# Kernel optimization log

Hardware: AMD Instinct MI355X
Metric: run time of the kernel (lower is better)

Reference implementation:

```python
import jax, jax.numpy as jnp
import numpy as np

TAU = 0.5
EPS = 1e-8


def setup_inputs() -> dict:
    key = jax.random.key(0)
    k1, k2 = jax.random.split(key)
    N, D = 200000, 512
    z_pos = jax.random.normal(k1, (N, D), dtype=jnp.float32)
    W = jax.random.normal(k2, (D, D), dtype=jnp.float32) * (1.0 / np.sqrt(D))
    b = jnp.zeros((D,), dtype=jnp.float32)
    return {"z_pos": z_pos, "W": W, "b": b}


def reference(z_pos, W, b):
    # sample_centroid: softmax-weighted centroid (computed on detached embeddings)
    h = jax.lax.stop_gradient(z_pos)
    init_c = h.mean(axis=0)                              # [D]
    d2 = jnp.sum((h - init_c[None, :]) ** 2, axis=1)     # [N]
    w = jax.nn.softmax(-d2 / TAU)                        # [N]
    c = jnp.sum(h * w[:, None], axis=0)                  # [D]

    # SimNet: dist = 1 - cosine_similarity(proj(x), c)
    x_proj = z_pos @ W.T + b                             # [N, D]
    x_norm = jnp.maximum(jnp.linalg.norm(x_proj, axis=-1), EPS)  # [N]
    c_norm = jnp.maximum(jnp.linalg.norm(c), EPS)
    cos = (x_proj @ c) / (x_norm * c_norm)               # [N]
    dist = 1.0 - cos
    return dist
```

## Files before the change

### kernel.cpp

```cpp
#include <hip/hip_runtime.h>
#include <hip/hip_bf16.h>
#include <math.h>

#define DD 512
#define EPSF 1e-8f
#define BM 128
#define BK 32
#define FBIG 3.402823466e+38f

typedef __bf16 bf16_t;
typedef __bf16 bf16x4 __attribute__((ext_vector_type(4)));
typedef __bf16 bf16x8 __attribute__((ext_vector_type(8)));
typedef float f32x4 __attribute__((ext_vector_type(4)));

__global__ void k_convW(const float* __restrict__ W, bf16_t* __restrict__ Wb) {
    int i = blockIdx.x * blockDim.x + threadIdx.x;
    float4 v = ((const float4*)W)[i];
    bf16x4 o;
    o[0] = (bf16_t)v.x; o[1] = (bf16_t)v.y; o[2] = (bf16_t)v.z; o[3] = (bf16_t)v.w;
    ((bf16x4*)Wb)[i] = o;
}

__global__ void k_colsum(const float* __restrict__ z, float* __restrict__ part, int N) {
    int t = threadIdx.x;
    int b = blockIdx.x;
    int col4 = t & 127, sub = t >> 7;
    const float4* z4 = (const float4*)z;
    float4 acc = make_float4(0.f, 0.f, 0.f, 0.f);
    int npair = (N + 1) >> 1;
    #pragma unroll 2
    for (int p = b; p < npair; p += gridDim.x) {
        int r = p * 2 + sub;
        if (r < N) {
            float4 v = z4[(size_t)r * 128 + col4];
            acc.x += v.x; acc.y += v.y; acc.z += v.z; acc.w += v.w;
        }
    }
    __shared__ float4 sm[128];
    if (sub == 1) sm[col4] = acc;
    __syncthreads();
    if (sub == 0) {
        float4 o = sm[col4];
        acc.x += o.x; acc.y += o.y; acc.z += o.z; acc.w += o.w;
        ((float4*)(part + (size_t)b * DD))[col4] = acc;
    }
}

__global__ void k_wcolsum(const float* __restrict__ z, const float* __restrict__ d2,
                          const float* __restrict__ d2min, const float* __restrict__ sinvp,
                          float* __restrict__ part, int N) {
    int t = threadIdx.x;
    int b = blockIdx.x;
    int col4 = t & 127, sub = t >> 7;
    float m  = d2min[0];
    float is = sinvp[0];
    const float4* z4 = (const float4*)z;
    float4 acc = make_float4(0.f, 0.f, 0.f, 0.f);
    int npair = (N + 1) >> 1;
    #pragma unroll 2
    for (int p = b; p < npair; p += gridDim.x) {
        int r = p * 2 + sub;
        if (r < N) {
            float w = __expf(-2.0f * (d2[r] - m)) * is;
            float4 v = z4[(size_t)r * 128 + col4];
            acc.x += w * v.x; acc.y += w * v.y; acc.z += w * v.z; acc.w += w * v.w;
        }
    }
    __shared__ float4 sm[128];
    if (sub == 1) sm[col4] = acc;
    __syncthreads();
    if (sub == 0) {
        float4 o = sm[col4];
        acc.x += o.x; acc.y += o.y; acc.z += o.z; acc.w += o.w;
        ((float4*)(part + (size_t)b * DD))[col4] = acc;
    }
}

__global__ void k_reduce1024(const float* __restrict__ part, float* __restrict__ outv, float scale) {
    __shared__ float sm[256];
    int j = blockIdx.x;
    int t = threadIdx.x;
    float s = part[(size_t)t * DD + j] + part[(size_t)(t + 256) * DD + j]
            + part[(size_t)(t + 512) * DD + j] + part[(size_t)(t + 768) * DD + j];
    sm[t] = s;
    __syncthreads();
    for (int st = 128; st > 0; st >>= 1) {
        if (t < st) sm[t] += sm[t + st];
        __syncthreads();
    }
    if (t == 0) outv[j] = sm[0] * scale;
}

__global__ void k_d2s(const float* __restrict__ z, const float* __restrict__ cbar,
                      float* __restrict__ d2, float* __restrict__ mpart,
                      float* __restrict__ spart, int N) {
    int lane = threadIdx.x & 63;
    int wvid = threadIdx.x >> 6;
    int gw = (blockIdx.x * blockDim.x + threadIdx.x) >> 6;
    int nw = (gridDim.x * blockDim.x) >> 6;
    const float4* c4 = (const float4*)cbar;
    float4 ca = c4[lane];
    float4 cb = c4[lane + 64];
    float m = FBIG, s = 0.f;
    for (int r = gw; r < N; r += nw) {
        const float4* zr = (const float4*)(z + (size_t)r * DD);
        float4 a  = zr[lane];
        float4 bb = zr[lane + 64];
        float d, sum = 0.f;
        d = a.x  - ca.x; sum += d * d;
        d = a.y  - ca.y; sum += d * d;
        d = a.z  - ca.z; sum += d * d;
        d = a.w  - ca.w; sum += d * d;
        d = bb.x - cb.x; sum += d * d;
        d = bb.y - cb.y; sum += d * d;
        d = bb.z - cb.z; sum += d * d;
        d = bb.w - cb.w; sum += d * d;
        #pragma unroll
        for (int off = 1; off < 64; off <<= 1) sum += __shfl_xor(sum, off, 64);
        if (lane == 0) d2[r] = sum;
        float nm = fminf(m, sum);
        s = s * __expf(-2.0f * (m - nm)) + __expf(-2.0f * (sum - nm));
        m = nm;
    }
    __shared__ float smm[4], sms[4];
    if (lane == 0) { smm[wvid] = m; sms[wvid] = s; }
    __syncthreads();
    if (threadIdx.x == 0) {
        float M = smm[0];
        M = fminf(M, smm[1]); M = fminf(M, smm[2]); M = fminf(M, smm[3]);
        float S = 0.f;
        #pragma unroll
        for (int i = 0; i < 4; ++i) S += sms[i] * __expf(-2.0f * (smm[i] - M));
        mpart[blockIdx.x] = M;
        spart[blockIdx.x] = S;
    }
}

__global__ void k_combine(const float* __restrict__ mpart, const float* __restrict__ spart,
                          float* __restrict__ d2min, float* __restrict__ sinvp) {
    __shared__ float smm[256], sms[256];
    int t = threadIdx.x;
    float M = FBIG, S = 0.f;
    for (int i = t; i < 1024; i += 256) {
        float m2 = mpart[i], s2 = spart[i];
        float nm = fminf(M, m2);
        S = S * __expf(-2.0f * (M - nm)) + s2 * __expf(-2.0f * (m2 - nm));
        M = nm;
    }
    smm[t] = M; sms[t] = S;
    __syncthreads();
    for (int st = 128; st > 0; st >>= 1) {
        if (t < st) {
            float m2 = smm[t + st], s2 = sms[t + st];
            float nm = fminf(smm[t], m2);
            sms[t] = sms[t] * __expf(-2.0f * (smm[t] - nm)) + s2 * __expf(-2.0f * (m2 - nm));
            smm[t] = nm;
        }
        __syncthreads();
    }
    if (t == 0) { d2min[0] = smm[0]; sinvp[0] = 1.0f / sms[0]; }
}

__global__ void k_cnorm(const float* __restrict__ cvec, float* __restrict__ outp) {
    __shared__ float sm[512];
    float v = cvec[threadIdx.x];
    sm[threadIdx.x] = v * v;
    __syncthreads();
    for (int st = 256; st > 0; st >>= 1) {
        if (threadIdx.x < st) sm[threadIdx.x] += sm[threadIdx.x + st];
        __syncthreads();
    }
    if (threadIdx.x == 0) outp[0] = 1.0f / fmaxf(sqrtf(sm[0]), EPSF);
}

__global__ __launch_bounds__(512, 2) void k_gemm(
    const float* __restrict__ z, const bf16_t* __restrict__ Wb,
    const float* __restrict__ bvec, const float* __restrict__ cvec,
    const float* __restrict__ cninv, float* __restrict__ out, int N)
{
    __shared__ bf16_t As[2][BM * BK];
    __shared__ bf16_t Bs[2][DD * BK];
    __shared__ float psq[BM][4];
    __shared__ float pdt[BM][4];

    const int t    = threadIdx.x;
    const int lane = t & 63;
    const int wv   = t >> 6;
    const int wr   = wv >> 2;
    const int wc   = wv & 3;
    const int quad = lane >> 4;
    const int l15  = lane & 15;
    const int row0 = blockIdx.x * BM;

    const int ai = t >> 2;
    const int ak = (t & 3) * 8;
    const bool arow_ok = (row0 + ai) < N;
    const float4* zrow = (const float4*)(z + (size_t)(row0 + ai) * DD + ak);

    const bf16_t* bsrc = Wb + (size_t)(t >> 2) * DD + (t & 3) * 8;

    f32x4 acc[4][8];
    #pragma unroll
    for (int a = 0; a < 4; ++a)
        #pragma unroll
        for (int b = 0; b < 8; ++b) acc[a][b] = (f32x4){0.f, 0.f, 0.f, 0.f};

    #pragma unroll
    for (int q = 0; q < 4; ++q) {
        int ldsoff = __builtin_amdgcn_readfirstlane(q * 8192 + wv * 1024);
        __builtin_amdgcn_global_load_lds(
            (const __attribute__((address_space(1))) unsigned int*)(const void*)(bsrc + (size_t)q * 128 * DD),
            (__attribute__((address_space(3))) unsigned int*)(void*)((char*)&Bs[0][0] + ldsoff),
            16, 0, 0);
    }
    {
        float4 v0 = make_float4(0.f,0.f,0.f,0.f), v1 = v0;
        if (arow_ok) { v0 = zrow[0]; v1 = zrow[1]; }
        bf16x8 a8;
        a8[0]=(bf16_t)v0.x; a8[1]=(bf16_t)v0.y; a8[2]=(bf16_t)v0.z; a8[3]=(bf16_t)v0.w;
        a8[4]=(bf16_t)v1.x; a8[5]=(bf16_t)v1.y; a8[6]=(bf16_t)v1.z; a8[7]=(bf16_t)v1.w;
        *(bf16x8*)(&As[0][ai * BK + ak]) = a8;
    }
    asm volatile("s_waitcnt vmcnt(0)" ::: "memory");
    __syncthreads();

    #pragma unroll 1
    for (int kc2 = 0; kc2 < 16; ++kc2) {
        const int cur = kc2 & 1;
        const int nxt = cur ^ 1;
        float4 v0 = make_float4(0.f,0.f,0.f,0.f), v1 = v0;
        if (kc2 < 15) {
            const int kc = (kc2 + 1) * BK;
            #pragma unroll
            for (int q = 0; q < 4; ++q) {
                int ldsoff = __builtin_amdgcn_readfirstlane(q * 8192 + wv * 1024);
                __builtin_amdgcn_global_load_lds(
                    (const __attribute__((address_space(1))) unsigned int*)(const void*)(bsrc + (size_t)q * 128 * DD + kc),
                    (__attribute__((address_space(3))) unsigned int*)(void*)((char*)&Bs[nxt][0] + ldsoff),
                    16, 0, 0);
            }
            if (arow_ok) { v0 = zrow[kc >> 2]; v1 = zrow[(kc >> 2) + 1]; }
        }

        bf16x8 af[4];
        #pragma unroll
        for (int rt = 0; rt < 4; ++rt)
            af[rt] = *(const bf16x8*)(&As[cur][(wr * 64 + rt * 16 + l15) * BK + quad * 8]);
        #pragma unroll
        for (int ct = 0; ct < 8; ++ct) {
            bf16x8 bfv = *(const bf16x8*)(&Bs[cur][(wc * 128 + ct * 16 + l15) * BK + quad * 8]);
            #pragma unroll
            for (int rt = 0; rt < 4; ++rt)
                acc[rt][ct] = __builtin_amdgcn_mfma_f32_16x16x32_bf16(af[rt], bfv, acc[rt][ct], 0, 0, 0);
        }

        if (kc2 < 15) {
            bf16x8 a8;
            a8[0]=(bf16_t)v0.x; a8[1]=(bf16_t)v0.y; a8[2]=(bf16_t)v0.z; a8[3]=(bf16_t)v0.w;
            a8[4]=(bf16_t)v1.x; a8[5]=(bf16_t)v1.y; a8[6]=(bf16_t)v1.z; a8[7]=(bf16_t)v1.w;
            *(bf16x8*)(&As[nxt][ai * BK + ak]) = a8;
        }
        asm volatile("s_waitcnt vmcnt(0)" ::: "memory");
        __syncthreads();
    }

    float bc[8], cc[8];
    #pragma unroll
    for (int ct = 0; ct < 8; ++ct) {
        int col = wc * 128 + ct * 16 + l15;
        bc[ct] = bvec[col];
        cc[ct] = cvec[col];
    }
    #pragma unroll
    for (int rt = 0; rt < 4; ++rt) {
        #pragma unroll
        for (int rg = 0; rg < 4; ++rg) {
            float sq = 0.f, dt = 0.f;
            #pragma unroll
            for (int ct = 0; ct < 8; ++ct) {
                float x = acc[rt][ct][rg] + bc[ct];
                sq += x * x;
                dt += x * cc[ct];
            }
            #pragma unroll
            for (int off = 1; off < 16; off <<= 1) {
                sq += __shfl_xor(sq, off, 64);
                dt += __shfl_xor(dt, off, 64);
            }
            if (l15 == 0) {
                int rl = wr * 64 + rt * 16 + quad * 4 + rg;
                psq[rl][wc] = sq;
                pdt[rl][wc] = dt;
            }
        }
    }
    __syncthreads();
    if (t < BM) {
        int r = row0 + t;
        if (r < N) {
            float sq = psq[t][0] + psq[t][1] + psq[t][2] + psq[t][3];
            float dt = pdt[t][0] + pdt[t][1] + pdt[t][2] + pdt[t][3];
            float xi = 1.0f / fmaxf(sqrtf(sq), EPSF);
            out[r] = 1.0f - dt * xi * cninv[0];
        }
    }
}

extern "C" void kernel_launch(void* const* d_in, const int* in_sizes, int n_in,
                              void* d_out, int out_size, void* d_ws, size_t ws_size,
                              hipStream_t stream)
{
    const float* z = (const float*)d_in[0];
    const float* W = (const float*)d_in[1];
    const float* b = (const float*)d_in[2];
    float* out = (float*)d_out;
    int N = in_sizes[0] / DD;

    float* ws = (float*)d_ws;
    size_t off = 0;
    float* part  = ws + off; off += (size_t)1024 * DD;
    float* cbar  = ws + off; off += DD;
    float* d2    = ws + off; off += (size_t)N;
    float* mpart = ws + off; off += 1024;
    float* spart = ws + off; off += 1024;
    float* d2min = ws + off; off += 1;
    float* sinvp = ws + off; off += 1;
    float* cvec  = ws + off; off += DD;
    float* cninv = ws + off; off += 1;
    off = (off + 3) & ~(size_t)3;
    bf16_t* Wb   = (bf16_t*)(ws + off);

    k_convW<<<256, 256, 0, stream>>>(W, Wb);
    k_colsum<<<1024, 256, 0, stream>>>(z, part, N);
    k_reduce1024<<<DD, 256, 0, stream>>>(part, cbar, 1.0f / (float)N);
    k_d2s<<<1024, 256, 0, stream>>>(z, cbar, d2, mpart, spart, N);
    k_combine<<<1, 256, 0, stream>>>(mpart, spart, d2min, sinvp);
    k_wcolsum<<<1024, 256, 0, stream>>>(z, d2, d2min, sinvp, part, N);
    k_reduce1024<<<DD, 256, 0, stream>>>(part, cvec, 1.0f);
    k_cnorm<<<1, DD, 0, stream>>>(cvec, cninv);
    int nblk = (N + BM - 1) / BM;
    k_gemm<<<nblk, 512, 0, stream>>>(z, Wb, b, cvec, cninv, out, N);
}
```

Baseline: 931.4 us.

## Split GEMM over column tiles, add final reduce, contiguous row ranges for reductions

The GEMM now tiles 128x128 output blocks over a 2D grid (4 column tiles) with 256 threads, single-buffered LDS, and writes per-column-tile partial norms and dots that a new final kernel combines. Column-sum kernels process contiguous row chunks per block instead of striding over the grid. The d2 kernel now gives each 16-lane group its own row. Together these aim at better occupancy and memory locality, but each z row is now read and converted four times by the GEMM, and the double buffering is gone.

```diff
diff --git a/kernel.cpp b/kernel.cpp
--- a/kernel.cpp
+++ b/kernel.cpp
@@ -5,8 +5,10 @@
 #define DD 512
 #define EPSF 1e-8f
 #define BM 128
+#define BN 128
 #define BK 32
 #define FBIG 3.402823466e+38f
+#define NPAD 200064
 
 typedef __bf16 bf16_t;
 typedef __bf16 bf16x4 __attribute__((ext_vector_type(4)));
@@ -21,20 +23,17 @@
     ((bf16x4*)Wb)[i] = o;
 }
 
-__global__ void k_colsum(const float* __restrict__ z, float* __restrict__ part, int N) {
+__global__ void k_colsum(const float* __restrict__ z, float* __restrict__ part, int N, int rpb) {
     int t = threadIdx.x;
     int b = blockIdx.x;
     int col4 = t & 127, sub = t >> 7;
+    int r0 = b * rpb, r1 = min(r0 + rpb, N);
     const float4* z4 = (const float4*)z;
     float4 acc = make_float4(0.f, 0.f, 0.f, 0.f);
-    int npair = (N + 1) >> 1;
-    #pragma unroll 2
-    for (int p = b; p < npair; p += gridDim.x) {
-        int r = p * 2 + sub;
-        if (r < N) {
-            float4 v = z4[(size_t)r * 128 + col4];
-            acc.x += v.x; acc.y += v.y; acc.z += v.z; acc.w += v.w;
-        }
+    #pragma unroll 4
+    for (int r = r0 + sub; r < r1; r += 2) {
+        float4 v = z4[(size_t)r * 128 + col4];
+        acc.x += v.x; acc.y += v.y; acc.z += v.z; acc.w += v.w;
     }
     __shared__ float4 sm[128];
     if (sub == 1) sm[col4] = acc;
@@ -48,23 +47,20 @@
 
 __global__ void k_wcolsum(const float* __restrict__ z, const float* __restrict__ d2,
                           const float* __restrict__ d2min, const float* __restrict__ sinvp,
-                          float* __restrict__ part, int N) {
+                          float* __restrict__ part, int N, int rpb) {
     int t = threadIdx.x;
     int b = blockIdx.x;
     int col4 = t & 127, sub = t >> 7;
+    int r0 = b * rpb, r1 = min(r0 + rpb, N);
     float m  = d2min[0];
     float is = sinvp[0];
     const float4* z4 = (const float4*)z;
     float4 acc = make_float4(0.f, 0.f, 0.f, 0.f);
-    int npair = (N + 1) >> 1;
-    #pragma unroll 2
-    for (int p = b; p < npair; p += gridDim.x) {
-        int r = p * 2 + sub;
-        if (r < N) {
-            float w = __expf(-2.0f * (d2[r] - m)) * is;
-            float4 v = z4[(size_t)r * 128 + col4];
-            acc.x += w * v.x; acc.y += w * v.y; acc.z += w * v.z; acc.w += w * v.w;
-        }
+    #pragma unroll 4
+    for (int r = r0 + sub; r < r1; r += 2) {
+        float w = __expf(-2.0f * (d2[r] - m)) * is;
+        float4 v = z4[(size_t)r * 128 + col4];
+        acc.x += w * v.x; acc.y += w * v.y; acc.z += w * v.z; acc.w += w * v.w;
     }
     __shared__ float4 sm[128];
     if (sub == 1) sm[col4] = acc;
@@ -94,40 +90,49 @@
 __global__ void k_d2s(const float* __restrict__ z, const float* __restrict__ cbar,
                       float* __restrict__ d2, float* __restrict__ mpart,
                       float* __restrict__ spart, int N) {
-    int lane = threadIdx.x & 63;
-    int wvid = threadIdx.x >> 6;
-    int gw = (blockIdx.x * blockDim.x + threadIdx.x) >> 6;
-    int nw = (gridDim.x * blockDim.x) >> 6;
+    int t = threadIdx.x;
+    int lane = t & 63, wv = t >> 6;
+    int l15 = lane & 15, r4 = lane >> 4;
     const float4* c4 = (const float4*)cbar;
-    float4 ca = c4[lane];
-    float4 cb = c4[lane + 64];
+    float4 cf[8];
+    #pragma unroll
+    for (int q = 0; q < 8; ++q) cf[q] = c4[q * 16 + l15];
+    int gw = (blockIdx.x * 256 + t) >> 6;
+    int nw = (gridDim.x * 256) >> 6;
     float m = FBIG, s = 0.f;
-    for (int r = gw; r < N; r += nw) {
+    #pragma unroll 2
+    for (int r = gw * 4 + r4; r < N; r += nw * 4) {
         const float4* zr = (const float4*)(z + (size_t)r * DD);
-        float4 a  = zr[lane];
-        float4 bb = zr[lane + 64];
-        float d, sum = 0.f;
-        d = a.x  - ca.x; sum += d * d;
-        d = a.y  - ca.y; sum += d * d;
-        d = a.z  - ca.z; sum += d * d;
-        d = a.w  - ca.w; sum += d * d;
-        d = bb.x - cb.x; sum += d * d;
-        d = bb.y - cb.y; sum += d * d;
-        d = bb.z - cb.z; sum += d * d;
-        d = bb.w - cb.w; sum += d * d;
-        #pragma unroll
-        for (int off = 1; off < 64; off <<= 1) sum += __shfl_xor(sum, off, 64);
-        if (lane == 0) d2[r] = sum;
+        float sum = 0.f;
+        #pragma unroll
+        for (int q = 0; q < 8; ++q) {
+            float4 v = zr[q * 16 + l15];
+            float d;
+            d = v.x - cf[q].x; sum += d * d;
+            d = v.y - cf[q].y; sum += d * d;
+            d = v.z - cf[q].z; sum += d * d;
+            d = v.w - cf[q].w; sum += d * d;
+        }
+        #pragma unroll
+        for (int off = 1; off < 16; off <<= 1) sum += __shfl_xor(sum, off, 64);
+        if (l15 == 0) d2[r] = sum;
         float nm = fminf(m, sum);
         s = s * __expf(-2.0f * (m - nm)) + __expf(-2.0f * (sum - nm));
         m = nm;
     }
+    #pragma unroll
+    for (int off = 16; off < 64; off <<= 1) {
+        float m2 = __shfl_xor(m, off, 64);
+        float s2 = __shfl_xor(s, off, 64);
+        float nm = fminf(m, m2);
+        s = s * __expf(-2.0f * (m - nm)) + s2 * __expf(-2.0f * (m2 - nm));
+        m = nm;
+    }
     __shared__ float smm[4], sms[4];
-    if (lane == 0) { smm[wvid] = m; sms[wvid] = s; }
-    __syncthreads();
-    if (threadIdx.x == 0) {
-        float M = smm[0];
-        M = fminf(M, smm[1]); M = fminf(M, smm[2]); M = fminf(M, smm[3]);
+    if (lane == 0) { smm[wv] = m; sms[wv] = s; }
+    __syncthreads();
+    if (t == 0) {
+        float M = fminf(fminf(smm[0], smm[1]), fminf(smm[2], smm[3]));
         float S = 0.f;
         #pragma unroll
         for (int i = 0; i < 4; ++i) S += sms[i] * __expf(-2.0f * (smm[i] - M));
@@ -173,101 +178,84 @@
     if (threadIdx.x == 0) outp[0] = 1.0f / fmaxf(sqrtf(sm[0]), EPSF);
 }
 
-__global__ __launch_bounds__(512, 2) void k_gemm(
+__global__ __launch_bounds__(256, 3) void k_gemm(
     const float* __restrict__ z, const bf16_t* __restrict__ Wb,
     const float* __restrict__ bvec, const float* __restrict__ cvec,
-    const float* __restrict__ cninv, float* __restrict__ out, int N)
+    float* __restrict__ sqp, float* __restrict__ dtp, int N)
 {
-    __shared__ bf16_t As[2][BM * BK];
-    __shared__ bf16_t Bs[2][DD * BK];
-    __shared__ float psq[BM][4];
-    __shared__ float pdt[BM][4];
+    __shared__ bf16_t As[BM * BK];
+    __shared__ bf16_t Bs[BN * BK];
+    __shared__ float psq[BM][2];
+    __shared__ float pdt[BM][2];
 
     const int t    = threadIdx.x;
     const int lane = t & 63;
     const int wv   = t >> 6;
-    const int wr   = wv >> 2;
-    const int wc   = wv & 3;
+    const int wr   = wv >> 1;
+    const int wc   = wv & 1;
     const int quad = lane >> 4;
     const int l15  = lane & 15;
-    const int row0 = blockIdx.x * BM;
-
-    const int ai = t >> 2;
-    const int ak = (t & 3) * 8;
-    const bool arow_ok = (row0 + ai) < N;
-    const float4* zrow = (const float4*)(z + (size_t)(row0 + ai) * DD + ak);
-
-    const bf16_t* bsrc = Wb + (size_t)(t >> 2) * DD + (t & 3) * 8;
-
-    f32x4 acc[4][8];
+    const int cb   = blockIdx.x;
+    const int row0 = blockIdx.y * BM;
+
+    const int arow = t >> 1;
+    const int ah   = t & 1;
+    int rowe = row0 + arow; if (rowe >= N) rowe = N - 1;
+    const float4* zp4 = (const float4*)(z + (size_t)rowe * DD + ah * 16);
+
+    const bf16_t* bp = Wb + (size_t)(cb * BN + (t >> 2)) * DD + (t & 3) * 8;
+
+    f32x4 acc[4][4];
     #pragma unroll
     for (int a = 0; a < 4; ++a)
         #pragma unroll
-        for (int b = 0; b < 8; ++b) acc[a][b] = (f32x4){0.f, 0.f, 0.f, 0.f};
-
-    #pragma unroll
-    for (int q = 0; q < 4; ++q) {
-        int ldsoff = __builtin_amdgcn_readfirstlane(q * 8192 + wv * 1024);
-        __builtin_amdgcn_global_load_lds(
-            (const __attribute__((address_space(1))) unsigned int*)(const void*)(bsrc + (size_t)q * 128 * DD),
-            (__attribute__((address_space(3))) unsigned int*)(void*)((char*)&Bs[0][0] + ldsoff),
-            16, 0, 0);
-    }
-    {
-        float4 v0 = make_float4(0.f,0.f,0.f,0.f), v1 = v0;
-        if (arow_ok) { v0 = zrow[0]; v1 = zrow[1]; }
-        bf16x8 a8;
-        a8[0]=(bf16_t)v0.x; a8[1]=(bf16_t)v0.y; a8[2]=(bf16_t)v0.z; a8[3]=(bf16_t)v0.w;
-        a8[4]=(bf16_t)v1.x; a8[5]=(bf16_t)v1.y; a8[6]=(bf16_t)v1.z; a8[7]=(bf16_t)v1.w;
-        *(bf16x8*)(&As[0][ai * BK + ak]) = a8;
-    }
-    asm volatile("s_waitcnt vmcnt(0)" ::: "memory");
-    __syncthreads();
-
-    #pragma unroll 1
-    for (int kc2 = 0; kc2 < 16; ++kc2) {
-        const int cur = kc2 & 1;
-        const int nxt = cur ^ 1;
-        float4 v0 = make_float4(0.f,0.f,0.f,0.f), v1 = v0;
-        if (kc2 < 15) {
-            const int kc = (kc2 + 1) * BK;
-            #pragma unroll
-            for (int q = 0; q < 4; ++q) {
-                int ldsoff = __builtin_amdgcn_readfirstlane(q * 8192 + wv * 1024);
-                __builtin_amdgcn_global_load_lds(
-                    (const __attribute__((address_space(1))) unsigned int*)(const void*)(bsrc + (size_t)q * 128 * DD + kc),
-                    (__attribute__((address_space(3))) unsigned int*)(void*)((char*)&Bs[nxt][0] + ldsoff),
-                    16, 0, 0);
-            }
-            if (arow_ok) { v0 = zrow[kc >> 2]; v1 = zrow[(kc >> 2) + 1]; }
+        for (int b = 0; b < 4; ++b) acc[a][b] = (f32x4){0.f, 0.f, 0.f, 0.f};
+
+    float4 v0 = zp4[0], v1 = zp4[1], v2 = zp4[2], v3 = zp4[3];
+
+    for (int kc = 0; kc < DD; kc += BK) {
+        if (kc) __syncthreads();
+
+        #pragma unroll
+        for (int q = 0; q < 2; ++q) {
+            int ldsoff = __builtin_amdgcn_readfirstlane(q * 4096 + wv * 1024);
+            __builtin_amdgcn_global_load_lds(
+                (const __attribute__((address_space(1))) unsigned int*)(const void*)(bp + (size_t)q * 64 * DD + kc),
+                (__attribute__((address_space(3))) unsigned int*)(void*)((char*)Bs + ldsoff),
+                16, 0, 0);
+        }
+        bf16x8 lo, hi;
+        lo[0]=(bf16_t)v0.x; lo[1]=(bf16_t)v0.y; lo[2]=(bf16_t)v0.z; lo[3]=(bf16_t)v0.w;
+        lo[4]=(bf16_t)v1.x; lo[5]=(bf16_t)v1.y; lo[6]=(bf16_t)v1.z; lo[7]=(bf16_t)v1.w;
+        hi[0]=(bf16_t)v2.x; hi[1]=(bf16_t)v2.y; hi[2]=(bf16_t)v2.z; hi[3]=(bf16_t)v2.w;
+        hi[4]=(bf16_t)v3.x; hi[5]=(bf16_t)v3.y; hi[6]=(bf16_t)v3.z; hi[7]=(bf16_t)v3.w;
+        *(bf16x8*)(As + arow * BK + ah * 16)     = lo;
+        *(bf16x8*)(As + arow * BK + ah * 16 + 8) = hi;
+
+        __syncthreads();
+
+        if (kc + BK < DD) {
+            int kf = (kc + BK) >> 2;
+            v0 = zp4[kf]; v1 = zp4[kf + 1]; v2 = zp4[kf + 2]; v3 = zp4[kf + 3];
         }
 
         bf16x8 af[4];
         #pragma unroll
         for (int rt = 0; rt < 4; ++rt)
-            af[rt] = *(const bf16x8*)(&As[cur][(wr * 64 + rt * 16 + l15) * BK + quad * 8]);
-        #pragma unroll
-        for (int ct = 0; ct < 8; ++ct) {
-            bf16x8 bfv = *(const bf16x8*)(&Bs[cur][(wc * 128 + ct * 16 + l15) * BK + quad * 8]);
+            af[rt] = *(const bf16x8*)(As + (wr * 64 + rt * 16 + l15) * BK + quad * 8);
+        #pragma unroll
+        for (int ct = 0; ct < 4; ++ct) {
+            bf16x8 bfv = *(const bf16x8*)(Bs + (wc * 64 + ct * 16 + l15) * BK + quad * 8);
             #pragma unroll
             for (int rt = 0; rt < 4; ++rt)
                 acc[rt][ct] = __builtin_amdgcn_mfma_f32_16x16x32_bf16(af[rt], bfv, acc[rt][ct], 0, 0, 0);
         }
-
-        if (kc2 < 15) {
-            bf16x8 a8;
-            a8[0]=(bf16_t)v0.x; a8[1]=(bf16_t)v0.y; a8[2]=(bf16_t)v0.z; a8[3]=(bf16_t)v0.w;
-            a8[4]=(bf16_t)v1.x; a8[5]=(bf16_t)v1.y; a8[6]=(bf16_t)v1.z; a8[7]=(bf16_t)v1.w;
-            *(bf16x8*)(&As[nxt][ai * BK + ak]) = a8;
-        }
-        asm volatile("s_waitcnt vmcnt(0)" ::: "memory");
-        __syncthreads();
-    }
-
-    float bc[8], cc[8];
-    #pragma unroll
-    for (int ct = 0; ct < 8; ++ct) {
-        int col = wc * 128 + ct * 16 + l15;
+    }
+
+    float bc[4], cc[4];
+    #pragma unroll
+    for (int ct = 0; ct < 4; ++ct) {
+        int col = cb * BN + wc * 64 + ct * 16 + l15;
         bc[ct] = bvec[col];
         cc[ct] = cvec[col];
     }
@@ -277,7 +265,7 @@
         for (int rg = 0; rg < 4; ++rg) {
             float sq = 0.f, dt = 0.f;
             #pragma unroll
-            for (int ct = 0; ct < 8; ++ct) {
+            for (int ct = 0; ct < 4; ++ct) {
                 float x = acc[rt][ct][rg] + bc[ct];
                 sq += x * x;
                 dt += x * cc[ct];
@@ -298,11 +286,19 @@
     if (t < BM) {
         int r = row0 + t;
         if (r < N) {
-            float sq = psq[t][0] + psq[t][1] + psq[t][2] + psq[t][3];
-            float dt = pdt[t][0] + pdt[t][1] + pdt[t][2] + pdt[t][3];
-            float xi = 1.0f / fmaxf(sqrtf(sq), EPSF);
-            out[r] = 1.0f - dt * xi * cninv[0];
-        }
+            sqp[(size_t)cb * NPAD + r] = psq[t][0] + psq[t][1];
+            dtp[(size_t)cb * NPAD + r] = pdt[t][0] + pdt[t][1];
+        }
+    }
+}
+
+__global__ void k_final(const float* __restrict__ sqp, const float* __restrict__ dtp,
+                        const float* __restrict__ cninv, float* __restrict__ out, int N) {
+    int r = blockIdx.x * blockDim.x + threadIdx.x;
+    if (r < N) {
+        float sq = sqp[r] + sqp[NPAD + r] + sqp[2 * NPAD + r] + sqp[3 * NPAD + r];
+        float dt = dtp[r] + dtp[NPAD + r] + dtp[2 * NPAD + r] + dtp[3 * NPAD + r];
+        out[r] = 1.0f - dt * cninv[0] / fmaxf(sqrtf(sq), EPSF);
     }
 }
 
@@ -320,7 +316,7 @@
     size_t off = 0;
     float* part  = ws + off; off += (size_t)1024 * DD;
     float* cbar  = ws + off; off += DD;
-    float* d2    = ws + off; off += (size_t)N;
+    float* d2    = ws + off; off += (size_t)NPAD;
     float* mpart = ws + off; off += 1024;
     float* spart = ws + off; off += 1024;
     float* d2min = ws + off; off += 1;
@@ -328,16 +324,21 @@
     float* cvec  = ws + off; off += DD;
     float* cninv = ws + off; off += 1;
     off = (off + 3) & ~(size_t)3;
+    float* sqp   = ws + off; off += (size_t)4 * NPAD;
+    float* dtp   = ws + off; off += (size_t)4 * NPAD;
     bf16_t* Wb   = (bf16_t*)(ws + off);
 
+    int rpb = (N + 1023) / 1024;
+
     k_convW<<<256, 256, 0, stream>>>(W, Wb);
-    k_colsum<<<1024, 256, 0, stream>>>(z, part, N);
+    k_colsum<<<1024, 256, 0, stream>>>(z, part, N, rpb);
     k_reduce1024<<<DD, 256, 0, stream>>>(part, cbar, 1.0f / (float)N);
     k_d2s<<<1024, 256, 0, stream>>>(z, cbar, d2, mpart, spart, N);
     k_combine<<<1, 256, 0, stream>>>(mpart, spart, d2min, sinvp);
-    k_wcolsum<<<1024, 256, 0, stream>>>(z, d2, d2min, sinvp, part, N);
+    k_wcolsum<<<1024, 256, 0, stream>>>(z, d2, d2min, sinvp, part, N, rpb);
     k_reduce1024<<<DD, 256, 0, stream>>>(part, cvec, 1.0f);
     k_cnorm<<<1, DD, 0, stream>>>(cvec, cninv);
-    int nblk = (N + BM - 1) / BM;
-    k_gemm<<<nblk, 512, 0, stream>>>(z, Wb, b, cvec, cninv, out, N);
-}
+    dim3 grid(4, (N + BM - 1) / BM);
+    k_gemm<<<grid, 256, 0, stream>>>(z, Wb, b, cvec, sqp, dtp, N);
+    k_final<<<(N + 255) / 256, 256, 0, stream>>>(sqp, dtp, cninv, out, N);
+}
```

Result: no change. 935.9 us (+0.5%).
